# Performance work log

Hardware: AMD Instinct MI355X
Metric: run time of the kernel (lower is better)

Reference implementation:

```python
import jax, jax.numpy as jnp
import numpy as np
import math

# Module config (matches init_kwargs)
FILTERS = 128
OUT_FACTOR = 0.5
B, H, W, C = 64, 64, 64, 64
HC = int(math.ceil(H / 2))  # weight/crop height = 32
WC = int(math.ceil(W / 2))  # weight/crop width  = 32
R_MIN = int(math.ceil(H * (1 - OUT_FACTOR) / 2))  # 16
R_MAX = R_MIN + int(math.ceil(H * (1 - OUT_FACTOR)))  # 48
C_MIN = int(math.ceil(W * (1 - OUT_FACTOR) / 2))  # 16
C_MAX = C_MIN + int(math.ceil(W * (1 - OUT_FACTOR)))  # 48


def setup_inputs() -> dict:
    key = jax.random.key(0)
    k1, k2, k3 = jax.random.split(key, 3)
    x = jax.random.normal(k1, (B, 2, H, W, C), dtype=jnp.float32)
    # keras 'random_normal' initializer: stddev 0.05
    W_r = jax.random.normal(k2, (HC, WC, C, FILTERS), dtype=jnp.float32) * 0.05
    W_i = jax.random.normal(k3, (HC, WC, C, FILTERS), dtype=jnp.float32) * 0.05
    b_r = jnp.zeros((FILTERS,), dtype=jnp.float32)
    b_i = jnp.zeros((FILTERS,), dtype=jnp.float32)
    return {"x": x, "W_r": W_r, "W_i": W_i, "b_r": b_r, "b_i": b_i}


def reference(x, W_r, W_i, b_r, b_i):
    # Crop center region: (B, 2, HC, WC, C)
    sp = x[:, :, R_MIN:R_MAX, C_MIN:C_MAX, :]
    xr, xi = sp[:, 0], sp[:, 1]  # (B, HC, WC, C)
    # Locally-connected complex contraction over channels (per-pixel weights)
    rr = jnp.einsum('bhwc,hwcf->bhwf', xr, W_r)
    ii = jnp.einsum('bhwc,hwcf->bhwf', xi, W_i)
    ri = jnp.einsum('bhwc,hwcf->bhwf', xr, W_i)
    ir = jnp.einsum('bhwc,hwcf->bhwf', xi, W_r)
    r = rr - ii + b_r  # (B, HC, WC, F)
    i = ri + ir + b_i
    y = jnp.stack([r, i], axis=1)  # (B, 2, HC, WC, F)
    # CReLU: relu applied independently to real and imaginary parts
    return jax.nn.relu(y)
```

## Files before the change

kernel.cpp:

```cpp
#include <hip/hip_runtime.h>

typedef __attribute__((ext_vector_type(8))) short short8;
typedef __attribute__((ext_vector_type(4))) float f32x4;
typedef __attribute__((ext_vector_type(2))) unsigned u32x2;
typedef __attribute__((ext_vector_type(4))) unsigned u32x4;

#define XSTR 72

__device__ __forceinline__ unsigned f2bf(float f) {
    unsigned u = __float_as_uint(f);
    return (u + 0x7fffu + ((u >> 16) & 1u)) >> 16;
}
__device__ __forceinline__ unsigned pack2(float lo, float hi) {
    return f2bf(lo) | (f2bf(hi) << 16);
}

__global__ __launch_bounds__(256) void cplx_dot_kernel(
    const float* __restrict__ x, const float* __restrict__ Wr,
    const float* __restrict__ Wi, const float* __restrict__ br,
    const float* __restrict__ bi, float* __restrict__ out)
{
    __shared__ __align__(16) short sXr[64 * XSTR];
    __shared__ __align__(16) short sXi[64 * XSTR];
    __shared__ __align__(16) short sWr[128 * XSTR];
    __shared__ __align__(16) short sWi[128 * XSTR];

    const int bid = blockIdx.x;
    const int h = bid >> 5, w = bid & 31;
    const int t = threadIdx.x;

    #pragma unroll
    for (int i = 0; i < 4; ++i) {
        int idx = t + 256 * i;
        int b = idx >> 4, q = idx & 15;
        size_t g = ((((size_t)b * 2) * 64 + (16 + h)) * 64 + (16 + w)) * 64 + q * 4;
        f32x4 vr = *(const f32x4*)(x + g);
        f32x4 vi = *(const f32x4*)(x + g + (size_t)64 * 64 * 64);
        u32x2 pr, pi;
        pr[0] = pack2(vr[0], vr[1]); pr[1] = pack2(vr[2], vr[3]);
        pi[0] = pack2(vi[0], vi[1]); pi[1] = pack2(vi[2], vi[3]);
        *(u32x2*)&sXr[b * XSTR + q * 4] = pr;
        *(u32x2*)&sXi[b * XSTR + q * 4] = pi;
    }

    {
        const int g = t & 31, cg = t >> 5;
        const size_t wbase = (((size_t)h * 32 + w) * 64) * 128;
        f32x4 rr[8], ri[8];
        #pragma unroll
        for (int i = 0; i < 8; ++i) {
            size_t off = wbase + (size_t)(8 * cg + i) * 128 + 4 * g;
            rr[i] = *(const f32x4*)(Wr + off);
            ri[i] = *(const f32x4*)(Wi + off);
        }
        #pragma unroll
        for (int j = 0; j < 4; ++j) {
            u32x4 pr, pi;
            pr[0] = pack2(rr[0][j], rr[1][j]); pr[1] = pack2(rr[2][j], rr[3][j]);
            pr[2] = pack2(rr[4][j], rr[5][j]); pr[3] = pack2(rr[6][j], rr[7][j]);
            pi[0] = pack2(ri[0][j], ri[1][j]); pi[1] = pack2(ri[2][j], ri[3][j]);
            pi[2] = pack2(ri[4][j], ri[5][j]); pi[3] = pack2(ri[6][j], ri[7][j]);
            *(u32x4*)&sWr[(4 * g + j) * XSTR + 8 * cg] = pr;
            *(u32x4*)&sWi[(4 * g + j) * XSTR + 8 * cg] = pi;
        }
    }
    __syncthreads();

    const int wv = t >> 6, l = t & 63;
    const int lr = l & 15, lh = l >> 4;

    f32x4 accR[8], accI[8];
    #pragma unroll
    for (int ft = 0; ft < 8; ++ft) {
        #pragma unroll
        for (int j = 0; j < 4; ++j) { accR[ft][j] = 0.f; accI[ft][j] = 0.f; }
    }

    #pragma unroll
    for (int kk = 0; kk < 2; ++kk) {
        const int c0 = 32 * kk + 8 * lh;
        short8 ar = *(const short8*)&sXr[(16 * wv + lr) * XSTR + c0];
        short8 ai = *(const short8*)&sXi[(16 * wv + lr) * XSTR + c0];
        short8 an;
        #pragma unroll
        for (int j = 0; j < 8; ++j) an[j] = ai[j] ^ (short)0x8000;
        #pragma unroll
        for (int ft = 0; ft < 8; ++ft) {
            short8 wr_ = *(const short8*)&sWr[(16 * ft + lr) * XSTR + c0];
            short8 wi_ = *(const short8*)&sWi[(16 * ft + lr) * XSTR + c0];
            accR[ft] = __builtin_amdgcn_mfma_f32_16x16x32_bf16(ar, wr_, accR[ft], 0, 0, 0);
            accR[ft] = __builtin_amdgcn_mfma_f32_16x16x32_bf16(an, wi_, accR[ft], 0, 0, 0);
            accI[ft] = __builtin_amdgcn_mfma_f32_16x16x32_bf16(ar, wi_, accI[ft], 0, 0, 0);
            accI[ft] = __builtin_amdgcn_mfma_f32_16x16x32_bf16(ai, wr_, accI[ft], 0, 0, 0);
        }
    }

    #pragma unroll
    for (int ft = 0; ft < 8; ++ft) {
        const int fc = 16 * ft + lr;
        const float vbr = br[fc], vbi = bi[fc];
        #pragma unroll
        for (int j = 0; j < 4; ++j) {
            const int b = 16 * wv + 4 * lh + j;
            size_t o = ((((size_t)b * 2) * 32 + h) * 32 + w) * 128 + fc;
            out[o] = fmaxf(accR[ft][j] + vbr, 0.f);
            out[o + (size_t)32 * 32 * 128] = fmaxf(accI[ft][j] + vbi, 0.f);
        }
    }
}

extern "C" void kernel_launch(void* const* d_in, const int* in_sizes, int n_in,
                              void* d_out, int out_size, void* d_ws, size_t ws_size,
                              hipStream_t stream) {
    const float* x  = (const float*)d_in[0];
    const float* Wr = (const float*)d_in[1];
    const float* Wi = (const float*)d_in[2];
    const float* br = (const float*)d_in[3];
    const float* bi = (const float*)d_in[4];
    float* out = (float*)d_out;
    hipLaunchKernelGGL(cplx_dot_kernel, dim3(1024), dim3(256), 0, stream,
                       x, Wr, Wi, br, bi, out);
}
```

Before: 31.45 us.

## Drop LDS staging; load MFMA fragments directly to registers with double-buffered X

Removes all shared-memory staging and the block barrier. Each wave now owns 32 filters and keeps its weight fragments in registers, loaded straight from global memory with scalar strided loads. The X fragments for four batch tiles are read directly from global memory and double-buffered so loads overlap the MFMAs. The launch bound asks for three blocks per SIMD. The trade-off is that every wave re-reads X, weight loads become uncoalesced scalar 4-byte accesses, and register pressure rises.

```diff
diff --git a/kernel.cpp b/kernel.cpp
--- a/kernel.cpp
+++ b/kernel.cpp
@@ -2,10 +2,7 @@
 
 typedef __attribute__((ext_vector_type(8))) short short8;
 typedef __attribute__((ext_vector_type(4))) float f32x4;
-typedef __attribute__((ext_vector_type(2))) unsigned u32x2;
 typedef __attribute__((ext_vector_type(4))) unsigned u32x4;
-
-#define XSTR 72
 
 __device__ __forceinline__ unsigned f2bf(float f) {
     unsigned u = __float_as_uint(f);
@@ -15,98 +12,119 @@
     return f2bf(lo) | (f2bf(hi) << 16);
 }
 
-__global__ __launch_bounds__(256) void cplx_dot_kernel(
+__global__ __launch_bounds__(256, 3) void cplx_dot_kernel(
     const float* __restrict__ x, const float* __restrict__ Wr,
     const float* __restrict__ Wi, const float* __restrict__ br,
     const float* __restrict__ bi, float* __restrict__ out)
 {
-    __shared__ __align__(16) short sXr[64 * XSTR];
-    __shared__ __align__(16) short sXi[64 * XSTR];
-    __shared__ __align__(16) short sWr[128 * XSTR];
-    __shared__ __align__(16) short sWi[128 * XSTR];
-
     const int bid = blockIdx.x;
     const int h = bid >> 5, w = bid & 31;
     const int t = threadIdx.x;
-
-    #pragma unroll
-    for (int i = 0; i < 4; ++i) {
-        int idx = t + 256 * i;
-        int b = idx >> 4, q = idx & 15;
-        size_t g = ((((size_t)b * 2) * 64 + (16 + h)) * 64 + (16 + w)) * 64 + q * 4;
-        f32x4 vr = *(const f32x4*)(x + g);
-        f32x4 vi = *(const f32x4*)(x + g + (size_t)64 * 64 * 64);
-        u32x2 pr, pi;
-        pr[0] = pack2(vr[0], vr[1]); pr[1] = pack2(vr[2], vr[3]);
-        pi[0] = pack2(vi[0], vi[1]); pi[1] = pack2(vi[2], vi[3]);
-        *(u32x2*)&sXr[b * XSTR + q * 4] = pr;
-        *(u32x2*)&sXi[b * XSTR + q * 4] = pi;
-    }
-
-    {
-        const int g = t & 31, cg = t >> 5;
-        const size_t wbase = (((size_t)h * 32 + w) * 64) * 128;
-        f32x4 rr[8], ri[8];
-        #pragma unroll
-        for (int i = 0; i < 8; ++i) {
-            size_t off = wbase + (size_t)(8 * cg + i) * 128 + 4 * g;
-            rr[i] = *(const f32x4*)(Wr + off);
-            ri[i] = *(const f32x4*)(Wi + off);
-        }
-        #pragma unroll
-        for (int j = 0; j < 4; ++j) {
-            u32x4 pr, pi;
-            pr[0] = pack2(rr[0][j], rr[1][j]); pr[1] = pack2(rr[2][j], rr[3][j]);
-            pr[2] = pack2(rr[4][j], rr[5][j]); pr[3] = pack2(rr[6][j], rr[7][j]);
-            pi[0] = pack2(ri[0][j], ri[1][j]); pi[1] = pack2(ri[2][j], ri[3][j]);
-            pi[2] = pack2(ri[4][j], ri[5][j]); pi[3] = pack2(ri[6][j], ri[7][j]);
-            *(u32x4*)&sWr[(4 * g + j) * XSTR + 8 * cg] = pr;
-            *(u32x4*)&sWi[(4 * g + j) * XSTR + 8 * cg] = pi;
-        }
-    }
-    __syncthreads();
-
     const int wv = t >> 6, l = t & 63;
     const int lr = l & 15, lh = l >> 4;
+    const int f0 = 32 * wv;
 
-    f32x4 accR[8], accI[8];
-    #pragma unroll
-    for (int ft = 0; ft < 8; ++ft) {
+    short8 wfr[2][2], wfi[2][2];
+    {
+        const size_t wbase = ((size_t)(h * 32 + w) * 64) * 128;
         #pragma unroll
-        for (int j = 0; j < 4; ++j) { accR[ft][j] = 0.f; accI[ft][j] = 0.f; }
-    }
-
-    #pragma unroll
-    for (int kk = 0; kk < 2; ++kk) {
-        const int c0 = 32 * kk + 8 * lh;
-        short8 ar = *(const short8*)&sXr[(16 * wv + lr) * XSTR + c0];
-        short8 ai = *(const short8*)&sXi[(16 * wv + lr) * XSTR + c0];
-        short8 an;
-        #pragma unroll
-        for (int j = 0; j < 8; ++j) an[j] = ai[j] ^ (short)0x8000;
-        #pragma unroll
-        for (int ft = 0; ft < 8; ++ft) {
-            short8 wr_ = *(const short8*)&sWr[(16 * ft + lr) * XSTR + c0];
-            short8 wi_ = *(const short8*)&sWi[(16 * ft + lr) * XSTR + c0];
-            accR[ft] = __builtin_amdgcn_mfma_f32_16x16x32_bf16(ar, wr_, accR[ft], 0, 0, 0);
-            accR[ft] = __builtin_amdgcn_mfma_f32_16x16x32_bf16(an, wi_, accR[ft], 0, 0, 0);
-            accI[ft] = __builtin_amdgcn_mfma_f32_16x16x32_bf16(ar, wi_, accI[ft], 0, 0, 0);
-            accI[ft] = __builtin_amdgcn_mfma_f32_16x16x32_bf16(ai, wr_, accI[ft], 0, 0, 0);
+        for (int ft = 0; ft < 2; ++ft) {
+            const int f = f0 + 16 * ft + lr;
+            #pragma unroll
+            for (int kk = 0; kk < 2; ++kk) {
+                const int c0 = 32 * kk + 8 * lh;
+                u32x4 pr, pi;
+                #pragma unroll
+                for (int j = 0; j < 4; ++j) {
+                    float r0 = Wr[wbase + (size_t)(c0 + 2 * j) * 128 + f];
+                    float r1 = Wr[wbase + (size_t)(c0 + 2 * j + 1) * 128 + f];
+                    float i0 = Wi[wbase + (size_t)(c0 + 2 * j) * 128 + f];
+                    float i1 = Wi[wbase + (size_t)(c0 + 2 * j + 1) * 128 + f];
+                    pr[j] = pack2(r0, r1);
+                    pi[j] = pack2(i0, i1);
+                }
+                wfr[ft][kk] = __builtin_bit_cast(short8, pr);
+                wfi[ft][kk] = __builtin_bit_cast(short8, pi);
+            }
         }
     }
 
-    #pragma unroll
-    for (int ft = 0; ft < 8; ++ft) {
-        const int fc = 16 * ft + lr;
-        const float vbr = br[fc], vbi = bi[fc];
-        #pragma unroll
-        for (int j = 0; j < 4; ++j) {
-            const int b = 16 * wv + 4 * lh + j;
-            size_t o = ((((size_t)b * 2) * 32 + h) * 32 + w) * 128 + fc;
-            out[o] = fmaxf(accR[ft][j] + vbr, 0.f);
-            out[o + (size_t)32 * 32 * 128] = fmaxf(accI[ft][j] + vbi, 0.f);
-        }
+    const float vbr0 = br[f0 + lr], vbr1 = br[f0 + 16 + lr];
+    const float vbi0 = bi[f0 + lr], vbi1 = bi[f0 + 16 + lr];
+
+    const size_t gimg = (size_t)64 * 64 * 64;
+    const size_t oimg = (size_t)32 * 32 * 128;
+
+#define LOAD_X(VR, VI, MT)                                                          \
+    {                                                                               \
+        const size_t gx = ((((size_t)(16 * (MT) + lr) * 2) * 64 + (16 + h)) * 64    \
+                           + (16 + w)) * 64;                                        \
+        _Pragma("unroll")                                                           \
+        for (int kk = 0; kk < 2; ++kk) {                                            \
+            const int c0 = 32 * kk + 8 * lh;                                        \
+            VR[kk][0] = *(const f32x4*)(x + gx + c0);                               \
+            VR[kk][1] = *(const f32x4*)(x + gx + c0 + 4);                           \
+            VI[kk][0] = *(const f32x4*)(x + gx + gimg + c0);                        \
+            VI[kk][1] = *(const f32x4*)(x + gx + gimg + c0 + 4);                    \
+        }                                                                           \
     }
+
+#define STEP(VR, VI, MT)                                                            \
+    {                                                                               \
+        f32x4 accR[2], accI[2];                                                     \
+        _Pragma("unroll")                                                           \
+        for (int ft = 0; ft < 2; ++ft)                                              \
+            _Pragma("unroll")                                                       \
+            for (int j = 0; j < 4; ++j) { accR[ft][j] = 0.f; accI[ft][j] = 0.f; }   \
+        _Pragma("unroll")                                                           \
+        for (int kk = 0; kk < 2; ++kk) {                                            \
+            u32x4 par, pai;                                                         \
+            _Pragma("unroll")                                                       \
+            for (int p = 0; p < 2; ++p) {                                           \
+                par[2 * p]     = pack2(VR[kk][p][0], VR[kk][p][1]);                 \
+                par[2 * p + 1] = pack2(VR[kk][p][2], VR[kk][p][3]);                 \
+                pai[2 * p]     = pack2(VI[kk][p][0], VI[kk][p][1]);                 \
+                pai[2 * p + 1] = pack2(VI[kk][p][2], VI[kk][p][3]);                 \
+            }                                                                       \
+            short8 arf = __builtin_bit_cast(short8, par);                           \
+            short8 aif = __builtin_bit_cast(short8, pai);                           \
+            short8 anf;                                                             \
+            _Pragma("unroll")                                                       \
+            for (int j = 0; j < 8; ++j) anf[j] = aif[j] ^ (short)0x8000;            \
+            _Pragma("unroll")                                                       \
+            for (int ft = 0; ft < 2; ++ft) {                                        \
+                accR[ft] = __builtin_amdgcn_mfma_f32_16x16x32_bf16(arf, wfr[ft][kk], accR[ft], 0, 0, 0); \
+                accR[ft] = __builtin_amdgcn_mfma_f32_16x16x32_bf16(anf, wfi[ft][kk], accR[ft], 0, 0, 0); \
+                accI[ft] = __builtin_amdgcn_mfma_f32_16x16x32_bf16(arf, wfi[ft][kk], accI[ft], 0, 0, 0); \
+                accI[ft] = __builtin_amdgcn_mfma_f32_16x16x32_bf16(aif, wfr[ft][kk], accI[ft], 0, 0, 0); \
+            }                                                                       \
+        }                                                                           \
+        _Pragma("unroll")                                                           \
+        for (int ft = 0; ft < 2; ++ft) {                                            \
+            const int fc = f0 + 16 * ft + lr;                                       \
+            const float bR = ft ? vbr1 : vbr0, bI = ft ? vbi1 : vbi0;               \
+            _Pragma("unroll")                                                       \
+            for (int j = 0; j < 4; ++j) {                                           \
+                const int b = 16 * (MT) + 4 * lh + j;                               \
+                size_t o = ((((size_t)b * 2) * 32 + h) * 32 + w) * 128 + fc;        \
+                out[o] = fmaxf(accR[ft][j] + bR, 0.f);                              \
+                out[o + oimg] = fmaxf(accI[ft][j] + bI, 0.f);                       \
+            }                                                                       \
+        }                                                                           \
+    }
+
+    f32x4 xrA[2][2], xiA[2][2], xrB[2][2], xiB[2][2];
+    LOAD_X(xrA, xiA, 0)
+    LOAD_X(xrB, xiB, 1)
+    STEP(xrA, xiA, 0)
+    LOAD_X(xrA, xiA, 2)
+    STEP(xrB, xiB, 1)
+    LOAD_X(xrB, xiB, 3)
+    STEP(xrA, xiA, 2)
+    STEP(xrB, xiB, 3)
+
+#undef LOAD_X
+#undef STEP
 }
 
 extern "C" void kernel_launch(void* const* d_in, const int* in_sizes, int n_in,
```

After: 43.54 us. +38.4%, slower.
